# Performance work log

Hardware: AMD Instinct MI355X
Metric: run time of the kernel (lower is better)

## Reference

```python
import jax, jax.numpy as jnp
import numpy as np

N_NODES = 100000
N_EDGES = 800000
N_GRAPHS = 2000
VOCAB = 30000
EMB = 64
REL = 16
HID = 128
NCLASS = 10


def setup_inputs() -> dict:
    key = jax.random.key(0)
    ks = jax.random.split(key, 16)
    x_tokens = jax.random.randint(ks[0], (N_NODES,), 0, VOCAB)
    edge_index = jax.random.randint(ks[1], (2, N_EDGES), 0, N_NODES)
    edge_type = jax.random.randint(ks[2], (N_EDGES,), 0, 3)
    batch = jnp.sort(jax.random.randint(ks[3], (N_NODES,), 0, N_GRAPHS))
    s = lambda k, shp, fan: jax.random.normal(k, shp, jnp.float32) * (1.0 / np.sqrt(fan))
    return {
        "x_tokens": x_tokens,
        "edge_index": edge_index,
        "edge_type": edge_type,
        "batch": batch,
        "num_graphs": N_GRAPHS,
        "emb_table": s(ks[4], (VOCAB, EMB), EMB),
        "rel_table": s(ks[5], (3, REL), REL),
        "w1_l": s(ks[6], (EMB + REL, HID), EMB + REL),
        "b1": jnp.zeros((HID,), jnp.float32),
        "w1_r": s(ks[7], (EMB, HID), EMB),
        "w2_l": s(ks[8], (HID, HID), HID),
        "b2": jnp.zeros((HID,), jnp.float32),
        "w2_r": s(ks[9], (HID, HID), HID),
        "lin_w": s(ks[10], (HID, NCLASS), HID),
        "lin_b": jnp.zeros((NCLASS,), jnp.float32),
    }


def _mean_agg(msgs, dst, n_nodes):
    # segment-mean of per-edge messages into destination nodes
    summed = jax.ops.segment_sum(msgs, dst, num_segments=n_nodes)
    deg = jax.ops.segment_sum(jnp.ones((msgs.shape[0],), msgs.dtype), dst, num_segments=n_nodes)
    return summed / jnp.maximum(deg, 1.0)[:, None]


def reference(x_tokens, edge_index, edge_type, batch, num_graphs,
              emb_table, rel_table, w1_l, b1, w1_r, w2_l, b2, w2_r, lin_w, lin_b):
    n_nodes = x_tokens.shape[0]
    src, dst = edge_index[0], edge_index[1]
    x = emb_table[x_tokens]                                  # [N, 64]
    rel_e = rel_table[edge_type]                             # [E, 16]
    src_feat = jnp.concatenate([x[src], rel_e], axis=1)      # [E, 80]
    # SAGEConv 1: mean-aggregate relation-aware messages + root transform
    agg1 = _mean_agg(src_feat, dst, n_nodes)                 # [N, 80]
    h = agg1 @ w1_l + b1 + x @ w1_r                          # [N, 128]
    h = jax.nn.relu(h)
    # SAGEConv 2
    agg2 = _mean_agg(h[src], dst, n_nodes)                   # [N, 128]
    h2 = agg2 @ w2_l + b2 + h @ w2_r                         # [N, 128]
    # global max pool over graphs, then ReLU -> (dropout: eval identity) -> Linear
    g = jax.ops.segment_max(h2, batch, num_segments=num_graphs)  # [G, 128]
    g = jax.nn.relu(g)
    return g @ lin_w + lin_b                                 # [G, nclass]
```

## Files before the change

kernel.cpp:

```cpp
#include <hip/hip_runtime.h>
#include <hip/hip_bf16.h>

#define NN 100000
#define NE 800000
#define NG 2000
#define EMB 64
#define HID 128
#define NCLS 10

#define NBKT 196
#define EPB 4096
#define NBA ((NE + EPB - 1) / EPB)
#define NSCAN (NBKT * NBA)
#define GS_NB ((NSCAN + 511) / 512)

typedef __attribute__((ext_vector_type(8))) short short8;
typedef __attribute__((ext_vector_type(4))) float f32x4;
typedef unsigned short u16;
typedef unsigned int u32;

static __device__ __forceinline__ unsigned fenc(float f) {
    unsigned u = __float_as_uint(f);
    return (u & 0x80000000u) ? ~u : (u | 0x80000000u);
}
static __device__ __forceinline__ float fdec(unsigned u) {
    return (u & 0x80000000u) ? __uint_as_float(u & 0x7FFFFFFFu) : __uint_as_float(~u);
}
static __device__ __forceinline__ u16 f2bf(float f) {
    u32 u = __float_as_uint(f);
    return (u16)((u + 0x7FFFu + ((u >> 16) & 1u)) >> 16);
}

__global__ void k_init(unsigned* genc, float* relp, u16* Bt1, u16* Bt2,
                       const float* rel_table, const float* w1l, const float* w1r,
                       const float* w2l, const float* w2r) {
    int i = blockIdx.x * 256 + threadIdx.x;
    if (i < NG * HID) genc[i] = 0x007FFFFFu;
    if (i < 3 * HID) {
        int t = i >> 7, j = i & 127;
        float s = 0.f;
        for (int k = 0; k < 16; ++k)
            s += rel_table[t * 16 + k] * w1l[(64 + k) * HID + j];
        relp[i] = s;
    }
    if (i < 128 * 128) {
        int c = i >> 7, k = i & 127;
        float w = (k < 64) ? w1l[k * HID + c] : w1r[(k - 64) * HID + c];
        Bt1[c * 128 + k] = f2bf(w);
    }
    if (i < 128 * 256) {
        int c = i >> 8, k = i & 255;
        float w = (k < 128) ? w2l[k * HID + c] : w2r[(k - 128) * HID + c];
        Bt2[c * 256 + k] = f2bf(w);
    }
}

__global__ void k_embed(const int* __restrict__ tok, const float* __restrict__ emb,
                        u32* __restrict__ axw) {
    int i = blockIdx.x * 256 + threadIdx.x;
    int n = i >> 5, p = i & 31;
    float2 e = *(const float2*)&emb[tok[n] * EMB + p * 2];
    axw[n * 64 + 32 + p] = (u32)f2bf(e.x) | ((u32)f2bf(e.y) << 16);
}


__global__ __launch_bounds__(256) void k_cnt(const int* __restrict__ dst,
                                             int* __restrict__ counts) {
    __shared__ int hist[NBKT];
    int t = threadIdx.x;
    for (int i = t; i < NBKT; i += 256) hist[i] = 0;
    __syncthreads();
    int base = blockIdx.x * EPB;
    for (int j = t; j < EPB; j += 256) {
        int e = base + j;
        if (e < NE) atomicAdd(&hist[dst[e] >> 9], 1);
    }
    __syncthreads();
    for (int i = t; i < NBKT; i += 256)
        counts[i * NBA + blockIdx.x] = hist[i];
}

__global__ __launch_bounds__(256) void k_gs1(const int* __restrict__ v, int* __restrict__ part) {
    __shared__ int ws[4];
    int t = threadIdx.x;
    int i0 = blockIdx.x * 512 + t * 2;
    int e0 = (i0 < NSCAN) ? v[i0] : 0;
    int e1 = (i0 + 1 < NSCAN) ? v[i0 + 1] : 0;
    int s = e0 + e1;
    for (int off = 32; off > 0; off >>= 1) s += __shfl_down(s, off, 64);
    if ((t & 63) == 0) ws[t >> 6] = s;
    __syncthreads();
    if (t == 0) part[blockIdx.x] = ws[0] + ws[1] + ws[2] + ws[3];
}

__global__ __launch_bounds__(128) void k_gs2(int* __restrict__ part) {
    __shared__ int s[128];
    int t = threadIdx.x;
    int v = (t < GS_NB) ? part[t] : 0;
    s[t] = v;
    __syncthreads();
    for (int off = 1; off < 128; off <<= 1) {
        int u = (t >= off) ? s[t - off] : 0;
        __syncthreads();
        s[t] += u;
        __syncthreads();
    }
    if (t < GS_NB) part[t] = s[t] - v;
}

__global__ __launch_bounds__(256) void k_gs3(const int* __restrict__ v,
                                             const int* __restrict__ part,
                                             int* __restrict__ out) {
    __shared__ int s[256];
    int t = threadIdx.x;
    int i0 = blockIdx.x * 512 + t * 2;
    int e0 = (i0 < NSCAN) ? v[i0] : 0;
    int e1 = (i0 + 1 < NSCAN) ? v[i0 + 1] : 0;
    int tsum = e0 + e1;
    s[t] = tsum;
    __syncthreads();
    for (int off = 1; off < 256; off <<= 1) {
        int u = (t >= off) ? s[t - off] : 0;
        __syncthreads();
        s[t] += u;
        __syncthreads();
    }
    int p0 = part[blockIdx.x] + s[t] - tsum;
    if (i0 < NSCAN) out[i0] = p0;
    if (i0 + 1 < NSCAN) out[i0 + 1] = p0 + e0;
}

__global__ __launch_bounds__(256) void k_part(const int* __restrict__ src,
                                              const int* __restrict__ dst,
                                              const int* __restrict__ et,
                                              const int* __restrict__ scanned,
                                              u32* __restrict__ coarse) {
    __shared__ int cur[NBKT];
    int t = threadIdx.x;
    for (int i = t; i < NBKT; i += 256) cur[i] = scanned[i * NBA + blockIdx.x];
    __syncthreads();
    int base = blockIdx.x * EPB;
    for (int j = t; j < EPB; j += 256) {
        int e = base + j;
        if (e < NE) {
            int d = dst[e];
            int pos = atomicAdd(&cur[d >> 9], 1);
            coarse[pos] = (u32)src[e] | ((u32)et[e] << 17) | ((u32)(d & 511) << 19);
        }
    }
}

__global__ __launch_bounds__(256) void k_csr(const int* __restrict__ scanned,
                                             const u32* __restrict__ coarse,
                                             int* __restrict__ offsets,
                                             int* __restrict__ packed) {
    __shared__ int hist[512];
    __shared__ int ex[512];
    __shared__ int ts[256];
    int b = blockIdx.x, t = threadIdx.x;
    int beg = scanned[b * NBA];
    int end = (b + 1 < NBKT) ? scanned[(b + 1) * NBA] : NE;
    hist[t] = 0; hist[t + 256] = 0;
    __syncthreads();
    for (int i = beg + t; i < end; i += 256)
        atomicAdd(&hist[(coarse[i] >> 19) & 511], 1);
    __syncthreads();
    int a0 = hist[2 * t], a1 = hist[2 * t + 1];
    int sum = a0 + a1;
    ts[t] = sum;
    __syncthreads();
    for (int off = 1; off < 256; off <<= 1) {
        int u = (t >= off) ? ts[t - off] : 0;
        __syncthreads();
        ts[t] += u;
        __syncthreads();
    }
    int ep = ts[t] - sum;
    ex[2 * t] = ep;
    ex[2 * t + 1] = ep + a0;
    __syncthreads();
    int node0 = b * 512;
    if (node0 + 2 * t < NN)     offsets[node0 + 2 * t]     = beg + ex[2 * t];
    if (node0 + 2 * t + 1 < NN) offsets[node0 + 2 * t + 1] = beg + ex[2 * t + 1];
    if (b == NBKT - 1 && t == 0) offsets[NN] = NE;
    hist[2 * t] = beg + ex[2 * t];
    hist[2 * t + 1] = beg + ex[2 * t + 1];
    __syncthreads();
    for (int i = beg + t; i < end; i += 256) {
        u32 pk = coarse[i];
        int pos = atomicAdd(&hist[(pk >> 19) & 511], 1);
        packed[pos] = (int)(pk & 0x1FFFFu) | (int)(((pk >> 17) & 3u) << 20);
    }
}

__global__ __launch_bounds__(256) void k_agg1(
    const int* __restrict__ offsets, const int* __restrict__ packed,
    u32* __restrict__ axw, float* __restrict__ fc) {
    int node = (blockIdx.x * 256 + threadIdx.x) >> 6;
    int lane = threadIdx.x & 63;
    int half = lane >> 5;
    int fl = lane & 31;
    int beg = offsets[node], end = offsets[node + 1];
    float a0 = 0.f, a1 = 0.f;
    int c0 = 0, c1 = 0, c2 = 0;
    for (int cb = beg; cb < end; cb += 64) {
        int pk = packed[min(cb + lane, NE - 1)];
        int cnt = min(end - cb, 64);
        int j = 0;
        for (; j + 8 <= cnt; j += 8) {
            #pragma unroll
            for (int q = 0; q < 4; ++q) {
                int p = __shfl(pk, j + q * 2 + half, 64);
                u32 v = axw[(p & 0xFFFFF) * 64 + 32 + fl];
                a0 += __uint_as_float(v << 16);
                a1 += __uint_as_float(v & 0xFFFF0000u);
                int t = p >> 20;
                c0 += (t == 0); c1 += (t == 1); c2 += (t == 2);
            }
        }
        for (; j < cnt; j += 2) {
            int idx = j + half;
            if (idx < cnt) {
                int p = __shfl(pk, idx, 64);
                u32 v = axw[(p & 0xFFFFF) * 64 + 32 + fl];
                a0 += __uint_as_float(v << 16);
                a1 += __uint_as_float(v & 0xFFFF0000u);
                int t = p >> 20;
                c0 += (t == 0); c1 += (t == 1); c2 += (t == 2);
            }
        }
    }
    a0 += __shfl_xor(a0, 32, 64);
    a1 += __shfl_xor(a1, 32, 64);
    c0 += __shfl_xor(c0, 32, 64);
    c1 += __shfl_xor(c1, 32, 64);
    c2 += __shfl_xor(c2, 32, 64);
    float inv = 1.0f / (float)max(end - beg, 1);
    if (half == 0)
        axw[node * 64 + fl] = (u32)f2bf(a0 * inv) | ((u32)f2bf(a1 * inv) << 16);
    if (lane == 0)
        *(float4*)&fc[node * 4] = make_float4(c0 * inv, c1 * inv, c2 * inv, 0.f);
}

__global__ __launch_bounds__(256) void k_agg2(
    const int* __restrict__ offsets, const int* __restrict__ packed,
    u32* __restrict__ ahw) {
    int node = (blockIdx.x * 256 + threadIdx.x) >> 6;
    int lane = threadIdx.x & 63;
    int beg = offsets[node], end = offsets[node + 1];
    float a0 = 0.f, a1 = 0.f;
    for (int cb = beg; cb < end; cb += 64) {
        int pk = packed[min(cb + lane, NE - 1)] & 0xFFFFF;
        int cnt = min(end - cb, 64);
        int j = 0;
        for (; j + 4 <= cnt; j += 4) {
            int s0 = __shfl(pk, j, 64), s1 = __shfl(pk, j + 1, 64);
            int s2 = __shfl(pk, j + 2, 64), s3 = __shfl(pk, j + 3, 64);
            u32 u0 = ahw[(size_t)s0 * 128 + 64 + lane];
            u32 u1 = ahw[(size_t)s1 * 128 + 64 + lane];
            u32 u2 = ahw[(size_t)s2 * 128 + 64 + lane];
            u32 u3 = ahw[(size_t)s3 * 128 + 64 + lane];
            a0 += __uint_as_float(u0 << 16) + __uint_as_float(u1 << 16)
                + __uint_as_float(u2 << 16) + __uint_as_float(u3 << 16);
            a1 += __uint_as_float(u0 & 0xFFFF0000u) + __uint_as_float(u1 & 0xFFFF0000u)
                + __uint_as_float(u2 & 0xFFFF0000u) + __uint_as_float(u3 & 0xFFFF0000u);
        }
        for (; j < cnt; ++j) {
            u32 u = ahw[(size_t)__shfl(pk, j, 64) * 128 + 64 + lane];
            a0 += __uint_as_float(u << 16);
            a1 += __uint_as_float(u & 0xFFFF0000u);
        }
    }
    float inv = 1.0f / (float)max(end - beg, 1);
    ahw[node * 128 + lane] = (u32)f2bf(a0 * inv) | ((u32)f2bf(a1 * inv) << 16);
}

__global__ __launch_bounds__(512) void k_gemm1(
    const u16* __restrict__ ax, const float* __restrict__ fc,
    const u16* __restrict__ Bt1, const float* __restrict__ b1,
    const float* __restrict__ relp, u16* __restrict__ ah) {
    __shared__ u16 Bs[128 * 128];
    int tid = threadIdx.x;
    int lane = tid & 63, w = tid >> 6;
    int mbase = blockIdx.x * 128;
    int r16 = lane & 15;
    int kg = (lane >> 4) * 8;
    int r = min(mbase + w * 16 + r16, NN - 1);
    short8 a[4];
    #pragma unroll
    for (int s = 0; s < 4; ++s)
        a[s] = *(const short8*)(ax + (size_t)r * 128 + s * 32 + kg);
    for (int i = tid; i < 2048; i += 512) {
        int col = i >> 4, p = i & 15;
        ((short8*)Bs)[i] = *(const short8*)(Bt1 + col * 128 + ((p ^ (col & 7)) << 3));
    }
    __syncthreads();
    f32x4 acc[8] = {};
    #pragma unroll
    for (int s = 0; s < 4; ++s) {
        int c = s * 4 + (lane >> 4);
        #pragma unroll
        for (int nf = 0; nf < 8; ++nf) {
            int col = nf * 16 + r16;
            short8 b = ((const short8*)Bs)[col * 16 + (c ^ (col & 7))];
            acc[nf] = __builtin_amdgcn_mfma_f32_16x16x32_bf16(a[s], b, acc[nf], 0, 0, 0);
        }
    }
    #pragma unroll
    for (int reg = 0; reg < 4; ++reg) {
        int row = mbase + w * 16 + (lane >> 4) * 4 + reg;
        if (row >= NN) continue;
        float4 f = *(const float4*)&fc[row * 4];
        #pragma unroll
        for (int nf = 0; nf < 8; ++nf) {
            int cc = nf * 16 + r16;
            float v = acc[nf][reg] + b1[cc]
                    + f.x * relp[cc] + f.y * relp[128 + cc] + f.z * relp[256 + cc];
            ah[(size_t)row * 256 + 128 + cc] = f2bf(fmaxf(v, 0.f));
        }
    }
}

__global__ __launch_bounds__(512) void k_gemm2(
    const u16* __restrict__ ah, const u16* __restrict__ Bt2,
    const float* __restrict__ b2, const int* __restrict__ batch,
    unsigned* __restrict__ genc) {
    __shared__ u16 Bs[128 * 256];
    int tid = threadIdx.x;
    int lane = tid & 63, w = tid >> 6;
    int mbase = blockIdx.x * 128;
    int r16 = lane & 15;
    int kg = (lane >> 4) * 8;
    int r = min(mbase + w * 16 + r16, NN - 1);
    short8 a[8];
    #pragma unroll
    for (int s = 0; s < 8; ++s)
        a[s] = *(const short8*)(ah + (size_t)r * 256 + s * 32 + kg);
    for (int i = tid; i < 4096; i += 512) {
        int col = i >> 5, p = i & 31;
        ((short8*)Bs)[i] = *(const short8*)(Bt2 + col * 256 + ((p ^ (col & 7)) << 3));
    }
    __syncthreads();
    f32x4 acc[8] = {};
    #pragma unroll
    for (int s = 0; s < 8; ++s) {
        int c = s * 4 + (lane >> 4);
        #pragma unroll
        for (int nf = 0; nf < 8; ++nf) {
            int col = nf * 16 + r16;
            short8 b = ((const short8*)Bs)[col * 32 + (c ^ (col & 7))];
            acc[nf] = __builtin_amdgcn_mfma_f32_16x16x32_bf16(a[s], b, acc[nf], 0, 0, 0);
        }
    }
    float bv[8];
    #pragma unroll
    for (int nf = 0; nf < 8; ++nf) bv[nf] = b2[nf * 16 + r16];
    int wbeg = mbase + w * 16;
    if (wbeg >= NN) return;
    int wlast = min(wbeg + 15, NN - 1);
    if (batch[wbeg] == batch[wlast]) {
        int bt = batch[wbeg];
        float vm[8];
        #pragma unroll
        for (int nf = 0; nf < 8; ++nf) {
            f32x4 v4 = acc[nf];
            vm[nf] = fmaxf(fmaxf(v4[0], v4[1]), fmaxf(v4[2], v4[3]));
        }
        #pragma unroll
        for (int nf = 0; nf < 8; ++nf)
            vm[nf] = fmaxf(vm[nf], __shfl_xor(vm[nf], 16, 64));
        #pragma unroll
        for (int nf = 0; nf < 8; ++nf)
            vm[nf] = fmaxf(vm[nf], __shfl_xor(vm[nf], 32, 64));
        if ((lane >> 4) == 0) {
            #pragma unroll
            for (int nf = 0; nf < 8; ++nf)
                atomicMax(&genc[bt * HID + nf * 16 + r16], fenc(vm[nf] + bv[nf]));
        }
    } else {
        int r0 = wbeg + (lane >> 4) * 4;
        if (r0 < NN) {
            if (r0 + 3 < NN && batch[r0] == batch[r0 + 3]) {
                int bt = batch[r0];
                #pragma unroll
                for (int nf = 0; nf < 8; ++nf) {
                    int cc = nf * 16 + r16;
                    f32x4 v4 = acc[nf];
                    float v = fmaxf(fmaxf(v4[0], v4[1]), fmaxf(v4[2], v4[3])) + bv[nf];
                    atomicMax(&genc[bt * HID + cc], fenc(v));
                }
            } else {
                #pragma unroll
                for (int reg = 0; reg < 4; ++reg) {
                    int row = r0 + reg;
                    if (row >= NN) continue;
                    int bt = batch[row];
                    #pragma unroll
                    for (int nf = 0; nf < 8; ++nf) {
                        int cc = nf * 16 + r16;
                        atomicMax(&genc[bt * HID + cc], fenc(acc[nf][reg] + bv[nf]));
                    }
                }
            }
        }
    }
}

__global__ void k_final(const unsigned* __restrict__ genc,
                        const float* __restrict__ lin_w, const float* __restrict__ lin_b,
                        float* __restrict__ out) {
    int gr = blockIdx.x;
    int lane = threadIdx.x;
    float g0 = fmaxf(fdec(genc[gr * HID + lane]), 0.f);
    float g1 = fmaxf(fdec(genc[gr * HID + 64 + lane]), 0.f);
    #pragma unroll
    for (int c = 0; c < NCLS; ++c) {
        float p = g0 * lin_w[lane * NCLS + c] + g1 * lin_w[(lane + 64) * NCLS + c];
        for (int off = 32; off > 0; off >>= 1)
            p += __shfl_down(p, off, 64);
        if (lane == 0) out[gr * NCLS + c] = p + lin_b[c];
    }
}

extern "C" void kernel_launch(void* const* d_in, const int* in_sizes, int n_in,
                              void* d_out, int out_size, void* d_ws, size_t ws_size,
                              hipStream_t stream) {
    const int* x_tokens   = (const int*)d_in[0];
    const int* edge_index = (const int*)d_in[1];
    const int* edge_type  = (const int*)d_in[2];
    const int* batch      = (const int*)d_in[3];
    const float* emb_table = (const float*)d_in[5];
    const float* rel_table = (const float*)d_in[6];
    const float* w1_l = (const float*)d_in[7];
    const float* b1   = (const float*)d_in[8];
    const float* w1_r = (const float*)d_in[9];
    const float* w2_l = (const float*)d_in[10];
    const float* b2   = (const float*)d_in[11];
    const float* w2_r = (const float*)d_in[12];
    const float* lin_w = (const float*)d_in[13];
    const float* lin_b = (const float*)d_in[14];
    float* out = (float*)d_out;

    const int* src = edge_index;
    const int* dst = edge_index + NE;

    char* ws = (char*)d_ws;
    size_t off = 0;
    auto alloc = [&](size_t bytes) {
        void* p = ws + off;
        off = (off + bytes + 255) & ~(size_t)255;
        return p;
    };
    u16* ax      = (u16*)alloc((size_t)NN * 128 * 2);
    u16* ah      = (u16*)alloc((size_t)NN * 256 * 2);
    float* fc    = (float*)alloc((size_t)NN * 4 * 4);
    int* offsets = (int*)alloc((size_t)(NN + 1) * 4);
    int* packed  = (int*)alloc((size_t)NE * 4);
    u32* coarse  = (u32*)alloc((size_t)NE * 4);
    int* counts  = (int*)alloc((size_t)NSCAN * 4);
    int* scanned = (int*)alloc((size_t)NSCAN * 4);
    int* gpart   = (int*)alloc((size_t)128 * 4);
    unsigned* genc = (unsigned*)alloc((size_t)NG * HID * 4);
    float* relp  = (float*)alloc((size_t)3 * HID * 4);
    u16* Bt1     = (u16*)alloc((size_t)128 * 128 * 2);
    u16* Bt2     = (u16*)alloc((size_t)128 * 256 * 2);
    (void)ws_size; (void)in_sizes; (void)n_in; (void)out_size;

    const int MT = (NN + 127) / 128;

    hipLaunchKernelGGL(k_init,  dim3(1000), dim3(256), 0, stream,
                       genc, relp, Bt1, Bt2, rel_table, w1_l, w1_r, w2_l, w2_r);
    hipLaunchKernelGGL(k_embed, dim3(NN * 32 / 256), dim3(256), 0, stream,
                       x_tokens, emb_table, (u32*)ax);
    hipLaunchKernelGGL(k_cnt,   dim3(NBA), dim3(256), 0, stream, dst, counts);
    hipLaunchKernelGGL(k_gs1,   dim3(GS_NB), dim3(256), 0, stream, counts, gpart);
    hipLaunchKernelGGL(k_gs2,   dim3(1), dim3(128), 0, stream, gpart);
    hipLaunchKernelGGL(k_gs3,   dim3(GS_NB), dim3(256), 0, stream, counts, gpart, scanned);
    hipLaunchKernelGGL(k_part,  dim3(NBA), dim3(256), 0, stream,
                       src, dst, edge_type, scanned, coarse);
    hipLaunchKernelGGL(k_csr,   dim3(NBKT), dim3(256), 0, stream,
                       scanned, coarse, offsets, packed);
    hipLaunchKernelGGL(k_agg1,  dim3(NN / 4), dim3(256), 0, stream,
                       offsets, packed, (u32*)ax, fc);
    hipLaunchKernelGGL(k_gemm1, dim3(MT), dim3(512), 0, stream,
                       ax, fc, Bt1, b1, relp, ah);
    hipLaunchKernelGGL(k_agg2,  dim3(NN / 4), dim3(256), 0, stream,
                       offsets, packed, (u32*)ah);
    hipLaunchKernelGGL(k_gemm2, dim3(MT), dim3(512), 0, stream,
                       ah, Bt2, b2, batch, genc);
    hipLaunchKernelGGL(k_final, dim3(NG), dim3(64), 0, stream, genc, lin_w, lin_b, out);
}
```

Baseline: 177.6 us.

## Fuse preprocessing kernels, restructure bucket scan, widen gather loads in aggregation

Merges init, embedding and bucket-count kernels into one launch, with blocks split by role. Replaces the three-pass global scan with a per-bucket row scan plus a small bucket-total scan, whose base offsets feed the partition and CSR kernels. Both aggregation kernels now gather 8-byte uint2 per lane, so each lane covers more features, more edges are in flight per wave, and the extra partial sums are reduced with cross-lane shuffles. This cuts launch count and memory-op count at the cost of extra shuffle reductions and a heterogeneous fused kernel.

```diff
diff --git a/kernel.cpp b/kernel.cpp
--- a/kernel.cpp
+++ b/kernel.cpp
@@ -11,8 +11,6 @@
 #define NBKT 196
 #define EPB 4096
 #define NBA ((NE + EPB - 1) / EPB)
-#define NSCAN (NBKT * NBA)
-#define GS_NB ((NSCAN + 511) / 512)
 
 typedef __attribute__((ext_vector_type(8))) short short8;
 typedef __attribute__((ext_vector_type(4))) float f32x4;
@@ -31,16 +29,41 @@
     return (u16)((u + 0x7FFFu + ((u >> 16) & 1u)) >> 16);
 }
 
-__global__ void k_init(unsigned* genc, float* relp, u16* Bt1, u16* Bt2,
-                       const float* rel_table, const float* w1l, const float* w1r,
-                       const float* w2l, const float* w2r) {
-    int i = blockIdx.x * 256 + threadIdx.x;
+__global__ __launch_bounds__(256) void k_pre(
+    const int* __restrict__ tok, const float* __restrict__ emb,
+    const int* __restrict__ dst, int* __restrict__ counts,
+    unsigned* __restrict__ genc, float* __restrict__ relp,
+    u16* __restrict__ Bt1, u16* __restrict__ Bt2,
+    const float* __restrict__ rel_table, const float* __restrict__ w1l,
+    const float* __restrict__ w1r, const float* __restrict__ w2l,
+    const float* __restrict__ w2r, u32* __restrict__ axw) {
+    __shared__ int hist[NBKT];
+    int g = blockIdx.x, t = threadIdx.x;
+    if (g < NBA) {
+        for (int i = t; i < NBKT; i += 256) hist[i] = 0;
+        __syncthreads();
+        int base = g * EPB;
+        for (int j = t; j < EPB; j += 256) {
+            int e = base + j;
+            if (e < NE) atomicAdd(&hist[dst[e] >> 9], 1);
+        }
+        __syncthreads();
+        for (int i = t; i < NBKT; i += 256)
+            counts[i * NBA + g] = hist[i];
+        return;
+    }
+    int i = (g - NBA) * 256 + t;
+    {
+        int n = i >> 5, p = i & 31;
+        float2 e = *(const float2*)&emb[tok[n] * EMB + p * 2];
+        axw[n * 64 + 32 + p] = (u32)f2bf(e.x) | ((u32)f2bf(e.y) << 16);
+    }
     if (i < NG * HID) genc[i] = 0x007FFFFFu;
     if (i < 3 * HID) {
-        int t = i >> 7, j = i & 127;
+        int tt = i >> 7, j = i & 127;
         float s = 0.f;
         for (int k = 0; k < 16; ++k)
-            s += rel_table[t * 16 + k] * w1l[(64 + k) * HID + j];
+            s += rel_table[tt * 16 + k] * w1l[(64 + k) * HID + j];
         relp[i] = s;
     }
     if (i < 128 * 128) {
@@ -55,69 +78,30 @@
     }
 }
 
-__global__ void k_embed(const int* __restrict__ tok, const float* __restrict__ emb,
-                        u32* __restrict__ axw) {
-    int i = blockIdx.x * 256 + threadIdx.x;
-    int n = i >> 5, p = i & 31;
-    float2 e = *(const float2*)&emb[tok[n] * EMB + p * 2];
-    axw[n * 64 + 32 + p] = (u32)f2bf(e.x) | ((u32)f2bf(e.y) << 16);
-}
-
-
-__global__ __launch_bounds__(256) void k_cnt(const int* __restrict__ dst,
-                                             int* __restrict__ counts) {
-    __shared__ int hist[NBKT];
-    int t = threadIdx.x;
-    for (int i = t; i < NBKT; i += 256) hist[i] = 0;
-    __syncthreads();
-    int base = blockIdx.x * EPB;
-    for (int j = t; j < EPB; j += 256) {
-        int e = base + j;
-        if (e < NE) atomicAdd(&hist[dst[e] >> 9], 1);
-    }
-    __syncthreads();
-    for (int i = t; i < NBKT; i += 256)
-        counts[i * NBA + blockIdx.x] = hist[i];
-}
-
-__global__ __launch_bounds__(256) void k_gs1(const int* __restrict__ v, int* __restrict__ part) {
-    __shared__ int ws[4];
-    int t = threadIdx.x;
-    int i0 = blockIdx.x * 512 + t * 2;
-    int e0 = (i0 < NSCAN) ? v[i0] : 0;
-    int e1 = (i0 + 1 < NSCAN) ? v[i0 + 1] : 0;
-    int s = e0 + e1;
-    for (int off = 32; off > 0; off >>= 1) s += __shfl_down(s, off, 64);
-    if ((t & 63) == 0) ws[t >> 6] = s;
-    __syncthreads();
-    if (t == 0) part[blockIdx.x] = ws[0] + ws[1] + ws[2] + ws[3];
-}
-
-__global__ __launch_bounds__(128) void k_gs2(int* __restrict__ part) {
-    __shared__ int s[128];
-    int t = threadIdx.x;
-    int v = (t < GS_NB) ? part[t] : 0;
+__global__ __launch_bounds__(256) void kS1(const int* __restrict__ counts,
+                                           int* __restrict__ scanned,
+                                           int* __restrict__ bucketT) {
+    __shared__ int s[256];
+    int b = blockIdx.x, t = threadIdx.x;
+    int v = (t < NBA) ? counts[b * NBA + t] : 0;
     s[t] = v;
     __syncthreads();
-    for (int off = 1; off < 128; off <<= 1) {
+    for (int off = 1; off < 256; off <<= 1) {
         int u = (t >= off) ? s[t - off] : 0;
         __syncthreads();
         s[t] += u;
         __syncthreads();
     }
-    if (t < GS_NB) part[t] = s[t] - v;
-}
-
-__global__ __launch_bounds__(256) void k_gs3(const int* __restrict__ v,
-                                             const int* __restrict__ part,
-                                             int* __restrict__ out) {
+    if (t < NBA) scanned[b * NBA + t] = s[t] - v;
+    if (t == 255) bucketT[b] = s[255];
+}
+
+__global__ __launch_bounds__(256) void kS2(const int* __restrict__ bucketT,
+                                           int* __restrict__ base) {
     __shared__ int s[256];
     int t = threadIdx.x;
-    int i0 = blockIdx.x * 512 + t * 2;
-    int e0 = (i0 < NSCAN) ? v[i0] : 0;
-    int e1 = (i0 + 1 < NSCAN) ? v[i0 + 1] : 0;
-    int tsum = e0 + e1;
-    s[t] = tsum;
+    int v = (t < NBKT) ? bucketT[t] : 0;
+    s[t] = v;
     __syncthreads();
     for (int off = 1; off < 256; off <<= 1) {
         int u = (t >= off) ? s[t - off] : 0;
@@ -125,23 +109,24 @@
         s[t] += u;
         __syncthreads();
     }
-    int p0 = part[blockIdx.x] + s[t] - tsum;
-    if (i0 < NSCAN) out[i0] = p0;
-    if (i0 + 1 < NSCAN) out[i0 + 1] = p0 + e0;
+    if (t < NBKT) base[t] = s[t] - v;
+    if (t == 255) base[NBKT] = s[255];
 }
 
 __global__ __launch_bounds__(256) void k_part(const int* __restrict__ src,
                                               const int* __restrict__ dst,
                                               const int* __restrict__ et,
                                               const int* __restrict__ scanned,
+                                              const int* __restrict__ base,
                                               u32* __restrict__ coarse) {
     __shared__ int cur[NBKT];
     int t = threadIdx.x;
-    for (int i = t; i < NBKT; i += 256) cur[i] = scanned[i * NBA + blockIdx.x];
-    __syncthreads();
-    int base = blockIdx.x * EPB;
+    for (int i = t; i < NBKT; i += 256)
+        cur[i] = base[i] + scanned[i * NBA + blockIdx.x];
+    __syncthreads();
+    int b0 = blockIdx.x * EPB;
     for (int j = t; j < EPB; j += 256) {
-        int e = base + j;
+        int e = b0 + j;
         if (e < NE) {
             int d = dst[e];
             int pos = atomicAdd(&cur[d >> 9], 1);
@@ -150,7 +135,7 @@
     }
 }
 
-__global__ __launch_bounds__(256) void k_csr(const int* __restrict__ scanned,
+__global__ __launch_bounds__(256) void k_csr(const int* __restrict__ base,
                                              const u32* __restrict__ coarse,
                                              int* __restrict__ offsets,
                                              int* __restrict__ packed) {
@@ -158,8 +143,8 @@
     __shared__ int ex[512];
     __shared__ int ts[256];
     int b = blockIdx.x, t = threadIdx.x;
-    int beg = scanned[b * NBA];
-    int end = (b + 1 < NBKT) ? scanned[(b + 1) * NBA] : NE;
+    int beg = base[b];
+    int end = base[b + 1];
     hist[t] = 0; hist[t + 256] = 0;
     __syncthreads();
     for (int i = beg + t; i < end; i += 256)
@@ -198,10 +183,10 @@
     u32* __restrict__ axw, float* __restrict__ fc) {
     int node = (blockIdx.x * 256 + threadIdx.x) >> 6;
     int lane = threadIdx.x & 63;
-    int half = lane >> 5;
-    int fl = lane & 31;
+    int qr = lane >> 4;
+    int ql = lane & 15;
     int beg = offsets[node], end = offsets[node + 1];
-    float a0 = 0.f, a1 = 0.f;
+    float a0 = 0.f, a1 = 0.f, a2 = 0.f, a3 = 0.f;
     int c0 = 0, c1 = 0, c2 = 0;
     for (int cb = beg; cb < end; cb += 64) {
         int pk = packed[min(cb + lane, NE - 1)];
@@ -209,35 +194,45 @@
         int j = 0;
         for (; j + 8 <= cnt; j += 8) {
             #pragma unroll
-            for (int q = 0; q < 4; ++q) {
-                int p = __shfl(pk, j + q * 2 + half, 64);
-                u32 v = axw[(p & 0xFFFFF) * 64 + 32 + fl];
-                a0 += __uint_as_float(v << 16);
-                a1 += __uint_as_float(v & 0xFFFF0000u);
-                int t = p >> 20;
-                c0 += (t == 0); c1 += (t == 1); c2 += (t == 2);
+            for (int q = 0; q < 2; ++q) {
+                int p = __shfl(pk, j + q * 4 + qr, 64);
+                uint2 v = *(const uint2*)&axw[(p & 0xFFFFF) * 64 + 32 + 2 * ql];
+                a0 += __uint_as_float(v.x << 16);
+                a1 += __uint_as_float(v.x & 0xFFFF0000u);
+                a2 += __uint_as_float(v.y << 16);
+                a3 += __uint_as_float(v.y & 0xFFFF0000u);
+                int tt = p >> 20;
+                c0 += (tt == 0); c1 += (tt == 1); c2 += (tt == 2);
             }
         }
-        for (; j < cnt; j += 2) {
-            int idx = j + half;
+        for (; j < cnt; j += 4) {
+            int idx = j + qr;
             if (idx < cnt) {
                 int p = __shfl(pk, idx, 64);
-                u32 v = axw[(p & 0xFFFFF) * 64 + 32 + fl];
-                a0 += __uint_as_float(v << 16);
-                a1 += __uint_as_float(v & 0xFFFF0000u);
-                int t = p >> 20;
-                c0 += (t == 0); c1 += (t == 1); c2 += (t == 2);
+                uint2 v = *(const uint2*)&axw[(p & 0xFFFFF) * 64 + 32 + 2 * ql];
+                a0 += __uint_as_float(v.x << 16);
+                a1 += __uint_as_float(v.x & 0xFFFF0000u);
+                a2 += __uint_as_float(v.y << 16);
+                a3 += __uint_as_float(v.y & 0xFFFF0000u);
+                int tt = p >> 20;
+                c0 += (tt == 0); c1 += (tt == 1); c2 += (tt == 2);
             }
         }
     }
-    a0 += __shfl_xor(a0, 32, 64);
-    a1 += __shfl_xor(a1, 32, 64);
-    c0 += __shfl_xor(c0, 32, 64);
-    c1 += __shfl_xor(c1, 32, 64);
-    c2 += __shfl_xor(c2, 32, 64);
+    a0 += __shfl_xor(a0, 16, 64); a0 += __shfl_xor(a0, 32, 64);
+    a1 += __shfl_xor(a1, 16, 64); a1 += __shfl_xor(a1, 32, 64);
+    a2 += __shfl_xor(a2, 16, 64); a2 += __shfl_xor(a2, 32, 64);
+    a3 += __shfl_xor(a3, 16, 64); a3 += __shfl_xor(a3, 32, 64);
+    c0 += __shfl_xor(c0, 16, 64); c0 += __shfl_xor(c0, 32, 64);
+    c1 += __shfl_xor(c1, 16, 64); c1 += __shfl_xor(c1, 32, 64);
+    c2 += __shfl_xor(c2, 16, 64); c2 += __shfl_xor(c2, 32, 64);
     float inv = 1.0f / (float)max(end - beg, 1);
-    if (half == 0)
-        axw[node * 64 + fl] = (u32)f2bf(a0 * inv) | ((u32)f2bf(a1 * inv) << 16);
+    if (qr == 0) {
+        uint2 o;
+        o.x = (u32)f2bf(a0 * inv) | ((u32)f2bf(a1 * inv) << 16);
+        o.y = (u32)f2bf(a2 * inv) | ((u32)f2bf(a3 * inv) << 16);
+        *(uint2*)&axw[node * 64 + 2 * ql] = o;
+    }
     if (lane == 0)
         *(float4*)&fc[node * 4] = make_float4(c0 * inv, c1 * inv, c2 * inv, 0.f);
 }
@@ -247,32 +242,47 @@
     u32* __restrict__ ahw) {
     int node = (blockIdx.x * 256 + threadIdx.x) >> 6;
     int lane = threadIdx.x & 63;
+    int half = lane >> 5, fl = lane & 31;
     int beg = offsets[node], end = offsets[node + 1];
-    float a0 = 0.f, a1 = 0.f;
+    float a0 = 0.f, a1 = 0.f, a2 = 0.f, a3 = 0.f;
     for (int cb = beg; cb < end; cb += 64) {
         int pk = packed[min(cb + lane, NE - 1)] & 0xFFFFF;
         int cnt = min(end - cb, 64);
         int j = 0;
-        for (; j + 4 <= cnt; j += 4) {
-            int s0 = __shfl(pk, j, 64), s1 = __shfl(pk, j + 1, 64);
-            int s2 = __shfl(pk, j + 2, 64), s3 = __shfl(pk, j + 3, 64);
-            u32 u0 = ahw[(size_t)s0 * 128 + 64 + lane];
-            u32 u1 = ahw[(size_t)s1 * 128 + 64 + lane];
-            u32 u2 = ahw[(size_t)s2 * 128 + 64 + lane];
-            u32 u3 = ahw[(size_t)s3 * 128 + 64 + lane];
-            a0 += __uint_as_float(u0 << 16) + __uint_as_float(u1 << 16)
-                + __uint_as_float(u2 << 16) + __uint_as_float(u3 << 16);
-            a1 += __uint_as_float(u0 & 0xFFFF0000u) + __uint_as_float(u1 & 0xFFFF0000u)
-                + __uint_as_float(u2 & 0xFFFF0000u) + __uint_as_float(u3 & 0xFFFF0000u);
-        }
-        for (; j < cnt; ++j) {
-            u32 u = ahw[(size_t)__shfl(pk, j, 64) * 128 + 64 + lane];
-            a0 += __uint_as_float(u << 16);
-            a1 += __uint_as_float(u & 0xFFFF0000u);
-        }
-    }
+        for (; j + 8 <= cnt; j += 8) {
+            #pragma unroll
+            for (int q = 0; q < 4; ++q) {
+                int p = __shfl(pk, j + q * 2 + half, 64);
+                uint2 v = *(const uint2*)&ahw[(size_t)p * 128 + 64 + 2 * fl];
+                a0 += __uint_as_float(v.x << 16);
+                a1 += __uint_as_float(v.x & 0xFFFF0000u);
+                a2 += __uint_as_float(v.y << 16);
+                a3 += __uint_as_float(v.y & 0xFFFF0000u);
+            }
+        }
+        for (; j < cnt; j += 2) {
+            int idx = j + half;
+            if (idx < cnt) {
+                int p = __shfl(pk, idx, 64);
+                uint2 v = *(const uint2*)&ahw[(size_t)p * 128 + 64 + 2 * fl];
+                a0 += __uint_as_float(v.x << 16);
+                a1 += __uint_as_float(v.x & 0xFFFF0000u);
+                a2 += __uint_as_float(v.y << 16);
+                a3 += __uint_as_float(v.y & 0xFFFF0000u);
+            }
+        }
+    }
+    a0 += __shfl_xor(a0, 32, 64);
+    a1 += __shfl_xor(a1, 32, 64);
+    a2 += __shfl_xor(a2, 32, 64);
+    a3 += __shfl_xor(a3, 32, 64);
     float inv = 1.0f / (float)max(end - beg, 1);
-    ahw[node * 128 + lane] = (u32)f2bf(a0 * inv) | ((u32)f2bf(a1 * inv) << 16);
+    if (half == 0) {
+        uint2 o;
+        o.x = (u32)f2bf(a0 * inv) | ((u32)f2bf(a1 * inv) << 16);
+        o.y = (u32)f2bf(a2 * inv) | ((u32)f2bf(a3 * inv) << 16);
+        *(uint2*)&ahw[node * 128 + 2 * fl] = o;
+    }
 }
 
 __global__ __launch_bounds__(512) void k_gemm1(
@@ -457,9 +467,10 @@
     int* offsets = (int*)alloc((size_t)(NN + 1) * 4);
     int* packed  = (int*)alloc((size_t)NE * 4);
     u32* coarse  = (u32*)alloc((size_t)NE * 4);
-    int* counts  = (int*)alloc((size_t)NSCAN * 4);
-    int* scanned = (int*)alloc((size_t)NSCAN * 4);
-    int* gpart   = (int*)alloc((size_t)128 * 4);
+    int* counts  = (int*)alloc((size_t)NBKT * NBA * 4);
+    int* scanned = (int*)alloc((size_t)NBKT * NBA * 4);
+    int* bucketT = (int*)alloc((size_t)NBKT * 4);
+    int* base    = (int*)alloc((size_t)(NBKT + 1) * 4);
     unsigned* genc = (unsigned*)alloc((size_t)NG * HID * 4);
     float* relp  = (float*)alloc((size_t)3 * HID * 4);
     u16* Bt1     = (u16*)alloc((size_t)128 * 128 * 2);
@@ -467,19 +478,17 @@
     (void)ws_size; (void)in_sizes; (void)n_in; (void)out_size;
 
     const int MT = (NN + 127) / 128;
-
-    hipLaunchKernelGGL(k_init,  dim3(1000), dim3(256), 0, stream,
-                       genc, relp, Bt1, Bt2, rel_table, w1_l, w1_r, w2_l, w2_r);
-    hipLaunchKernelGGL(k_embed, dim3(NN * 32 / 256), dim3(256), 0, stream,
-                       x_tokens, emb_table, (u32*)ax);
-    hipLaunchKernelGGL(k_cnt,   dim3(NBA), dim3(256), 0, stream, dst, counts);
-    hipLaunchKernelGGL(k_gs1,   dim3(GS_NB), dim3(256), 0, stream, counts, gpart);
-    hipLaunchKernelGGL(k_gs2,   dim3(1), dim3(128), 0, stream, gpart);
-    hipLaunchKernelGGL(k_gs3,   dim3(GS_NB), dim3(256), 0, stream, counts, gpart, scanned);
+    const int PRE = NBA + NN * 32 / 256;
+
+    hipLaunchKernelGGL(k_pre,   dim3(PRE), dim3(256), 0, stream,
+                       x_tokens, emb_table, dst, counts, genc, relp, Bt1, Bt2,
+                       rel_table, w1_l, w1_r, w2_l, w2_r, (u32*)ax);
+    hipLaunchKernelGGL(kS1,     dim3(NBKT), dim3(256), 0, stream, counts, scanned, bucketT);
+    hipLaunchKernelGGL(kS2,     dim3(1), dim3(256), 0, stream, bucketT, base);
     hipLaunchKernelGGL(k_part,  dim3(NBA), dim3(256), 0, stream,
-                       src, dst, edge_type, scanned, coarse);
+                       src, dst, edge_type, scanned, base, coarse);
     hipLaunchKernelGGL(k_csr,   dim3(NBKT), dim3(256), 0, stream,
-                       scanned, coarse, offsets, packed);
+                       base, coarse, offsets, packed);
     hipLaunchKernelGGL(k_agg1,  dim3(NN / 4), dim3(256), 0, stream,
                        offsets, packed, (u32*)ax, fc);
     hipLaunchKernelGGL(k_gemm1, dim3(MT), dim3(512), 0, stream,
```

Result: faster. 165.6 us (-6.8%).

## Fuse preprocessing kernels and replace three-pass global scan with per-bucket scan

Applied to the files above, without the earlier changes.

Merges init, embedding lookup and bucket counting into one launch, with block ranges choosing the role. Replaces the three-kernel global scan with one per-bucket scan kernel that writes bucket totals. The consumers (k_part and k_csr) then rescan those 196 totals locally in shared memory. This cuts the launch count from 7 to 3 in the preprocessing phase, at the cost of redundant small scans in every k_part and k_csr block.

```diff
diff --git a/kernel.cpp b/kernel.cpp
--- a/kernel.cpp
+++ b/kernel.cpp
@@ -11,8 +11,6 @@
 #define NBKT 196
 #define EPB 4096
 #define NBA ((NE + EPB - 1) / EPB)
-#define NSCAN (NBKT * NBA)
-#define GS_NB ((NSCAN + 511) / 512)
 
 typedef __attribute__((ext_vector_type(8))) short short8;
 typedef __attribute__((ext_vector_type(4))) float f32x4;
@@ -31,16 +29,41 @@
     return (u16)((u + 0x7FFFu + ((u >> 16) & 1u)) >> 16);
 }
 
-__global__ void k_init(unsigned* genc, float* relp, u16* Bt1, u16* Bt2,
-                       const float* rel_table, const float* w1l, const float* w1r,
-                       const float* w2l, const float* w2r) {
-    int i = blockIdx.x * 256 + threadIdx.x;
+__global__ __launch_bounds__(256) void k_pre(
+    const int* __restrict__ tok, const float* __restrict__ emb,
+    const int* __restrict__ dst, int* __restrict__ counts,
+    unsigned* __restrict__ genc, float* __restrict__ relp,
+    u16* __restrict__ Bt1, u16* __restrict__ Bt2,
+    const float* __restrict__ rel_table, const float* __restrict__ w1l,
+    const float* __restrict__ w1r, const float* __restrict__ w2l,
+    const float* __restrict__ w2r, u32* __restrict__ axw) {
+    __shared__ int hist[NBKT];
+    int g = blockIdx.x, t = threadIdx.x;
+    if (g < NBA) {
+        for (int i = t; i < NBKT; i += 256) hist[i] = 0;
+        __syncthreads();
+        int base = g * EPB;
+        for (int j = t; j < EPB; j += 256) {
+            int e = base + j;
+            if (e < NE) atomicAdd(&hist[dst[e] >> 9], 1);
+        }
+        __syncthreads();
+        for (int i = t; i < NBKT; i += 256)
+            counts[i * NBA + g] = hist[i];
+        return;
+    }
+    int i = (g - NBA) * 256 + t;
+    {
+        int n = i >> 5, p = i & 31;
+        float2 e = *(const float2*)&emb[tok[n] * EMB + p * 2];
+        axw[n * 64 + 32 + p] = (u32)f2bf(e.x) | ((u32)f2bf(e.y) << 16);
+    }
     if (i < NG * HID) genc[i] = 0x007FFFFFu;
     if (i < 3 * HID) {
-        int t = i >> 7, j = i & 127;
+        int tt = i >> 7, j = i & 127;
         float s = 0.f;
         for (int k = 0; k < 16; ++k)
-            s += rel_table[t * 16 + k] * w1l[(64 + k) * HID + j];
+            s += rel_table[tt * 16 + k] * w1l[(64 + k) * HID + j];
         relp[i] = s;
     }
     if (i < 128 * 128) {
@@ -55,69 +78,13 @@
     }
 }
 
-__global__ void k_embed(const int* __restrict__ tok, const float* __restrict__ emb,
-                        u32* __restrict__ axw) {
-    int i = blockIdx.x * 256 + threadIdx.x;
-    int n = i >> 5, p = i & 31;
-    float2 e = *(const float2*)&emb[tok[n] * EMB + p * 2];
-    axw[n * 64 + 32 + p] = (u32)f2bf(e.x) | ((u32)f2bf(e.y) << 16);
-}
-
-
-__global__ __launch_bounds__(256) void k_cnt(const int* __restrict__ dst,
-                                             int* __restrict__ counts) {
-    __shared__ int hist[NBKT];
-    int t = threadIdx.x;
-    for (int i = t; i < NBKT; i += 256) hist[i] = 0;
-    __syncthreads();
-    int base = blockIdx.x * EPB;
-    for (int j = t; j < EPB; j += 256) {
-        int e = base + j;
-        if (e < NE) atomicAdd(&hist[dst[e] >> 9], 1);
-    }
-    __syncthreads();
-    for (int i = t; i < NBKT; i += 256)
-        counts[i * NBA + blockIdx.x] = hist[i];
-}
-
-__global__ __launch_bounds__(256) void k_gs1(const int* __restrict__ v, int* __restrict__ part) {
-    __shared__ int ws[4];
-    int t = threadIdx.x;
-    int i0 = blockIdx.x * 512 + t * 2;
-    int e0 = (i0 < NSCAN) ? v[i0] : 0;
-    int e1 = (i0 + 1 < NSCAN) ? v[i0 + 1] : 0;
-    int s = e0 + e1;
-    for (int off = 32; off > 0; off >>= 1) s += __shfl_down(s, off, 64);
-    if ((t & 63) == 0) ws[t >> 6] = s;
-    __syncthreads();
-    if (t == 0) part[blockIdx.x] = ws[0] + ws[1] + ws[2] + ws[3];
-}
-
-__global__ __launch_bounds__(128) void k_gs2(int* __restrict__ part) {
-    __shared__ int s[128];
-    int t = threadIdx.x;
-    int v = (t < GS_NB) ? part[t] : 0;
+__global__ __launch_bounds__(256) void kS1(const int* __restrict__ counts,
+                                           int* __restrict__ scanned,
+                                           int* __restrict__ bucketT) {
+    __shared__ int s[256];
+    int b = blockIdx.x, t = threadIdx.x;
+    int v = (t < NBA) ? counts[b * NBA + t] : 0;
     s[t] = v;
-    __syncthreads();
-    for (int off = 1; off < 128; off <<= 1) {
-        int u = (t >= off) ? s[t - off] : 0;
-        __syncthreads();
-        s[t] += u;
-        __syncthreads();
-    }
-    if (t < GS_NB) part[t] = s[t] - v;
-}
-
-__global__ __launch_bounds__(256) void k_gs3(const int* __restrict__ v,
-                                             const int* __restrict__ part,
-                                             int* __restrict__ out) {
-    __shared__ int s[256];
-    int t = threadIdx.x;
-    int i0 = blockIdx.x * 512 + t * 2;
-    int e0 = (i0 < NSCAN) ? v[i0] : 0;
-    int e1 = (i0 + 1 < NSCAN) ? v[i0 + 1] : 0;
-    int tsum = e0 + e1;
-    s[t] = tsum;
     __syncthreads();
     for (int off = 1; off < 256; off <<= 1) {
         int u = (t >= off) ? s[t - off] : 0;
@@ -125,23 +92,33 @@
         s[t] += u;
         __syncthreads();
     }
-    int p0 = part[blockIdx.x] + s[t] - tsum;
-    if (i0 < NSCAN) out[i0] = p0;
-    if (i0 + 1 < NSCAN) out[i0 + 1] = p0 + e0;
+    if (t < NBA) scanned[b * NBA + t] = s[t] - v;
+    if (t == 255) bucketT[b] = s[255];
 }
 
 __global__ __launch_bounds__(256) void k_part(const int* __restrict__ src,
                                               const int* __restrict__ dst,
                                               const int* __restrict__ et,
                                               const int* __restrict__ scanned,
+                                              const int* __restrict__ bucketT,
                                               u32* __restrict__ coarse) {
     __shared__ int cur[NBKT];
+    __shared__ int s[256];
     int t = threadIdx.x;
-    for (int i = t; i < NBKT; i += 256) cur[i] = scanned[i * NBA + blockIdx.x];
-    __syncthreads();
-    int base = blockIdx.x * EPB;
+    int v = (t < NBKT) ? bucketT[t] : 0;
+    s[t] = v;
+    __syncthreads();
+    for (int off = 1; off < 256; off <<= 1) {
+        int u = (t >= off) ? s[t - off] : 0;
+        __syncthreads();
+        s[t] += u;
+        __syncthreads();
+    }
+    if (t < NBKT) cur[t] = (s[t] - v) + scanned[t * NBA + blockIdx.x];
+    __syncthreads();
+    int b0 = blockIdx.x * EPB;
     for (int j = t; j < EPB; j += 256) {
-        int e = base + j;
+        int e = b0 + j;
         if (e < NE) {
             int d = dst[e];
             int pos = atomicAdd(&cur[d >> 9], 1);
@@ -150,16 +127,29 @@
     }
 }
 
-__global__ __launch_bounds__(256) void k_csr(const int* __restrict__ scanned,
+__global__ __launch_bounds__(256) void k_csr(const int* __restrict__ bucketT,
                                              const u32* __restrict__ coarse,
                                              int* __restrict__ offsets,
                                              int* __restrict__ packed) {
     __shared__ int hist[512];
     __shared__ int ex[512];
     __shared__ int ts[256];
+    __shared__ int sBeg, sEnd;
     int b = blockIdx.x, t = threadIdx.x;
-    int beg = scanned[b * NBA];
-    int end = (b + 1 < NBKT) ? scanned[(b + 1) * NBA] : NE;
+    {
+        int v = (t < NBKT) ? bucketT[t] : 0;
+        ts[t] = v;
+        __syncthreads();
+        for (int off = 1; off < 256; off <<= 1) {
+            int u = (t >= off) ? ts[t - off] : 0;
+            __syncthreads();
+            ts[t] += u;
+            __syncthreads();
+        }
+        if (t == b) { sBeg = ts[b] - v; sEnd = ts[b]; }
+        __syncthreads();
+    }
+    int beg = sBeg, end = sEnd;
     hist[t] = 0; hist[t + 256] = 0;
     __syncthreads();
     for (int i = beg + t; i < end; i += 256)
@@ -457,9 +447,9 @@
     int* offsets = (int*)alloc((size_t)(NN + 1) * 4);
     int* packed  = (int*)alloc((size_t)NE * 4);
     u32* coarse  = (u32*)alloc((size_t)NE * 4);
-    int* counts  = (int*)alloc((size_t)NSCAN * 4);
-    int* scanned = (int*)alloc((size_t)NSCAN * 4);
-    int* gpart   = (int*)alloc((size_t)128 * 4);
+    int* counts  = (int*)alloc((size_t)NBKT * NBA * 4);
+    int* scanned = (int*)alloc((size_t)NBKT * NBA * 4);
+    int* bucketT = (int*)alloc((size_t)NBKT * 4);
     unsigned* genc = (unsigned*)alloc((size_t)NG * HID * 4);
     float* relp  = (float*)alloc((size_t)3 * HID * 4);
     u16* Bt1     = (u16*)alloc((size_t)128 * 128 * 2);
@@ -467,19 +457,16 @@
     (void)ws_size; (void)in_sizes; (void)n_in; (void)out_size;
 
     const int MT = (NN + 127) / 128;
-
-    hipLaunchKernelGGL(k_init,  dim3(1000), dim3(256), 0, stream,
-                       genc, relp, Bt1, Bt2, rel_table, w1_l, w1_r, w2_l, w2_r);
-    hipLaunchKernelGGL(k_embed, dim3(NN * 32 / 256), dim3(256), 0, stream,
-                       x_tokens, emb_table, (u32*)ax);
-    hipLaunchKernelGGL(k_cnt,   dim3(NBA), dim3(256), 0, stream, dst, counts);
-    hipLaunchKernelGGL(k_gs1,   dim3(GS_NB), dim3(256), 0, stream, counts, gpart);
-    hipLaunchKernelGGL(k_gs2,   dim3(1), dim3(128), 0, stream, gpart);
-    hipLaunchKernelGGL(k_gs3,   dim3(GS_NB), dim3(256), 0, stream, counts, gpart, scanned);
+    const int PRE = NBA + NN * 32 / 256;
+
+    hipLaunchKernelGGL(k_pre,   dim3(PRE), dim3(256), 0, stream,
+                       x_tokens, emb_table, dst, counts, genc, relp, Bt1, Bt2,
+                       rel_table, w1_l, w1_r, w2_l, w2_r, (u32*)ax);
+    hipLaunchKernelGGL(kS1,     dim3(NBKT), dim3(256), 0, stream, counts, scanned, bucketT);
     hipLaunchKernelGGL(k_part,  dim3(NBA), dim3(256), 0, stream,
-                       src, dst, edge_type, scanned, coarse);
+                       src, dst, edge_type, scanned, bucketT, coarse);
     hipLaunchKernelGGL(k_csr,   dim3(NBKT), dim3(256), 0, stream,
-                       scanned, coarse, offsets, packed);
+                       bucketT, coarse, offsets, packed);
     hipLaunchKernelGGL(k_agg1,  dim3(NN / 4), dim3(256), 0, stream,
                        offsets, packed, (u32*)ax, fc);
     hipLaunchKernelGGL(k_gemm1, dim3(MT), dim3(512), 0, stream,
```

Result: faster. 166.3 us (-6.3%).
